# Optimization experiments

Measured on AMD Instinct MI355X. Metric: run time of the kernel, lower is better.

Reference implementation:

```python
import jax, jax.numpy as jnp
import numpy as np

ALPHA, BETA, LMBD, GAMMA = 0.0005, 1.0, 1.0, 1.0
MARGIN, THRES = 100.0, 0.5
EPS = 1e-7


def _bce(p, t):
    p = jnp.clip(p, EPS, 1.0 - EPS)
    return -jnp.mean(t * jnp.log(p) + (1.0 - t) * jnp.log1p(-p))


def setup_inputs() -> dict:
    key = jax.random.key(0)
    ks = jax.random.split(key, 9)
    B, T, D, C = 16, 2048, 2048, 100
    return {
        "score_act": jax.random.uniform(ks[0], (B, C), jnp.float32),
        "score_bkg": jax.random.uniform(ks[1], (B, C), jnp.float32),
        "feat_act": jax.random.normal(ks[2], (B, T, D), jnp.float32),
        "feat_bkg": jax.random.normal(ks[3], (B, T, D), jnp.float32),
        "label": jax.random.uniform(ks[4], (B, C), jnp.float32),
        "gt": jax.random.uniform(ks[5], (B, T, C), jnp.float32),
        "sup_cas": jax.random.uniform(ks[6], (B, T, C), jnp.float32),
        "cas_s": jax.random.uniform(ks[7], (B, T, C), jnp.float32),
        "cas_t": jax.random.uniform(ks[8], (B, T, C), jnp.float32),
    }


def reference(score_act, score_bkg, feat_act, feat_bkg, label, gt, sup_cas, cas_s, cas_t):
    # classification BCE against normalized multi-label target
    label_n = label / jnp.sum(label, axis=1, keepdims=True)
    loss_cls = _bce(score_act, label_n)

    # background BCE against uniform 1/C target
    C = label.shape[1]
    loss_be = _bce(score_bkg, jnp.full_like(label, 1.0 / C))

    # uncertainty modeling: feature-magnitude margin loss
    act_norm = jnp.linalg.norm(jnp.mean(feat_act, axis=1), axis=1)  # [B]
    bkg_norm = jnp.linalg.norm(jnp.mean(feat_bkg, axis=1), axis=1)  # [B]
    loss_act = jnp.maximum(MARGIN - act_norm, 0.0)
    loss_um = jnp.mean((loss_act + bkg_norm) ** 2)

    # balanced_ce, vectorized over (batch, class): mean of L2 norms over time
    # for (i,j) slices that contain at least one positive snippet
    pmask = (gt > THRES).astype(sup_cas.dtype)            # [B,T,C]
    norms = jnp.linalg.norm(sup_cas - pmask, axis=1)      # [B,C]
    valid = jnp.sum(pmask, axis=1) > 0                    # [B,C]
    count = jnp.maximum(jnp.sum(valid), 1).astype(norms.dtype)
    loss_sup = jnp.sum(jnp.where(valid, norms, 0.0)) / count

    # student/teacher CAS MSE
    loss_st = jnp.mean((cas_s - cas_t) ** 2)

    loss_total = (loss_cls + ALPHA * loss_um + BETA * loss_be
                  + LMBD * loss_sup + GAMMA * loss_st)
    return jnp.stack([loss_total, loss_cls, loss_be, loss_um, loss_sup, loss_st])
```

## Files before the change

kernel.cpp:

```cpp
#include <hip/hip_runtime.h>
#include <cmath>

constexpr int B = 16, T = 2048, D = 2048, C = 100;
#define EPS_F 1e-7f

__global__ void colsum_kernel(const float* __restrict__ feat, float* __restrict__ out,
                              int rows_per_chunk) {
    const int b = blockIdx.z;
    const int d0 = (blockIdx.x * blockDim.x + threadIdx.x) * 4;
    const int t0 = blockIdx.y * rows_per_chunk;
    float4 acc = make_float4(0.f, 0.f, 0.f, 0.f);
    const float* base = feat + ((size_t)b * T + t0) * D + d0;
    for (int t = 0; t < rows_per_chunk; ++t) {
        float4 v = *reinterpret_cast<const float4*>(base + (size_t)t * D);
        acc.x += v.x; acc.y += v.y; acc.z += v.z; acc.w += v.w;
    }
    float* o = out + b * D + d0;
    atomicAdd(o + 0, acc.x);
    atomicAdd(o + 1, acc.y);
    atomicAdd(o + 2, acc.z);
    atomicAdd(o + 3, acc.w);
}

__global__ void sup_kernel(const float* __restrict__ gt, const float* __restrict__ sup,
                           float* __restrict__ sumsq, float* __restrict__ cnt,
                           int rows_per_chunk) {
    const int b = blockIdx.y;
    const int c = threadIdx.x;
    const int t0 = blockIdx.x * rows_per_chunk;
    if (c >= C) return;
    float acc = 0.f, pc = 0.f;
    size_t base = ((size_t)b * T + t0) * C + c;
    for (int t = 0; t < rows_per_chunk; ++t) {
        float g = gt[base + (size_t)t * C];
        float s = sup[base + (size_t)t * C];
        float m = (g > 0.5f) ? 1.f : 0.f;
        float d = s - m;
        acc += d * d;
        pc += m;
    }
    atomicAdd(&sumsq[b * C + c], acc);
    atomicAdd(&cnt[b * C + c], pc);
}

__global__ void st_kernel(const float4* __restrict__ s, const float4* __restrict__ t,
                          float* __restrict__ acc, int n4) {
    int idx = blockIdx.x * blockDim.x + threadIdx.x;
    int stride = gridDim.x * blockDim.x;
    float local = 0.f;
    for (int i = idx; i < n4; i += stride) {
        float4 a = s[i], b4 = t[i];
        float dx = a.x - b4.x, dy = a.y - b4.y, dz = a.z - b4.z, dw = a.w - b4.w;
        local += dx * dx + dy * dy + dz * dz + dw * dw;
    }
    for (int off = 32; off; off >>= 1) local += __shfl_down(local, off, 64);
    __shared__ float wsum[4];
    int lane = threadIdx.x & 63, wv = threadIdx.x >> 6;
    if (lane == 0) wsum[wv] = local;
    __syncthreads();
    if (threadIdx.x == 0) {
        atomicAdd(acc, wsum[0] + wsum[1] + wsum[2] + wsum[3]);
    }
}

__device__ __forceinline__ float block_reduce256(float v, float* sdata) {
    int tid = threadIdx.x;
    sdata[tid] = v;
    __syncthreads();
    for (int s = 128; s > 0; s >>= 1) {
        if (tid < s) sdata[tid] += sdata[tid + s];
        __syncthreads();
    }
    float r = sdata[0];
    __syncthreads();
    return r;
}

__global__ void final_kernel(const float* __restrict__ score_act,
                             const float* __restrict__ score_bkg,
                             const float* __restrict__ label,
                             const float* __restrict__ colsum_act,
                             const float* __restrict__ colsum_bkg,
                             const float* __restrict__ sup_sumsq,
                             const float* __restrict__ sup_cnt,
                             const float* __restrict__ st_acc,
                             float* __restrict__ out) {
    __shared__ float sdata[256];
    __shared__ float rowsum[B];
    __shared__ float an[B], bn[B];
    const int tid = threadIdx.x;
    const int N = B * C;

    if (tid < B) rowsum[tid] = 0.f;
    __syncthreads();
    for (int i = tid; i < N; i += 256) atomicAdd(&rowsum[i / C], label[i]);
    __syncthreads();

    float lc = 0.f;
    for (int i = tid; i < N; i += 256) {
        float tgt = label[i] / rowsum[i / C];
        float p = fminf(fmaxf(score_act[i], EPS_F), 1.f - EPS_F);
        lc -= tgt * logf(p) + (1.f - tgt) * log1pf(-p);
    }
    float loss_cls = block_reduce256(lc, sdata) / (float)N;

    float lb = 0.f;
    const float u = 1.f / (float)C;
    for (int i = tid; i < N; i += 256) {
        float p = fminf(fmaxf(score_bkg[i], EPS_F), 1.f - EPS_F);
        lb -= u * logf(p) + (1.f - u) * log1pf(-p);
    }
    float loss_be = block_reduce256(lb, sdata) / (float)N;

    const float invT = 1.f / (float)T;
    for (int b = 0; b < B; ++b) {
        float la = 0.f, lg = 0.f;
        for (int d = tid; d < D; d += 256) {
            float va = colsum_act[b * D + d] * invT;
            float vb = colsum_bkg[b * D + d] * invT;
            la += va * va;
            lg += vb * vb;
        }
        float sa = block_reduce256(la, sdata);
        float sb = block_reduce256(lg, sdata);
        if (tid == 0) { an[b] = sqrtf(sa); bn[b] = sqrtf(sb); }
    }
    __syncthreads();

    float ss = 0.f, sc = 0.f;
    for (int i = tid; i < N; i += 256) {
        if (sup_cnt[i] > 0.f) { ss += sqrtf(sup_sumsq[i]); sc += 1.f; }
    }
    float sup_sum = block_reduce256(ss, sdata);
    float sup_count = block_reduce256(sc, sdata);

    if (tid == 0) {
        float loss_um = 0.f;
        for (int b = 0; b < B; ++b) {
            float la = fmaxf(100.f - an[b], 0.f);
            float v = la + bn[b];
            loss_um += v * v;
        }
        loss_um /= (float)B;
        float loss_sup = sup_sum / fmaxf(sup_count, 1.f);
        float loss_st = *st_acc / (float)((size_t)B * T * C);
        float total = loss_cls + 0.0005f * loss_um + 1.0f * loss_be
                    + 1.0f * loss_sup + 1.0f * loss_st;
        out[0] = total;
        out[1] = loss_cls;
        out[2] = loss_be;
        out[3] = loss_um;
        out[4] = loss_sup;
        out[5] = loss_st;
    }
}

extern "C" void kernel_launch(void* const* d_in, const int* in_sizes, int n_in,
                              void* d_out, int out_size, void* d_ws, size_t ws_size,
                              hipStream_t stream) {
    const float* score_act = (const float*)d_in[0];
    const float* score_bkg = (const float*)d_in[1];
    const float* feat_act  = (const float*)d_in[2];
    const float* feat_bkg  = (const float*)d_in[3];
    const float* label     = (const float*)d_in[4];
    const float* gt        = (const float*)d_in[5];
    const float* sup_cas   = (const float*)d_in[6];
    const float* cas_s     = (const float*)d_in[7];
    const float* cas_t     = (const float*)d_in[8];
    float* out = (float*)d_out;
    float* ws  = (float*)d_ws;

    float* colsum_act = ws;
    float* colsum_bkg = ws + (size_t)B * D;
    float* sup_sumsq  = ws + (size_t)2 * B * D;
    float* sup_cnt    = sup_sumsq + B * C;
    float* st_acc     = sup_cnt + B * C;
    size_t ws_needed  = ((size_t)2 * B * D + 2 * B * C + 1) * sizeof(float);

    hipMemsetAsync(d_ws, 0, ws_needed, stream);

    {
        const int rows = 64;
        dim3 grid(D / (256 * 4), T / rows, B);
        colsum_kernel<<<grid, 256, 0, stream>>>(feat_act, colsum_act, rows);
        colsum_kernel<<<grid, 256, 0, stream>>>(feat_bkg, colsum_bkg, rows);
    }
    {
        const int rows = 32;
        dim3 grid(T / rows, B);
        sup_kernel<<<grid, 128, 0, stream>>>(gt, sup_cas, sup_sumsq, sup_cnt, rows);
    }
    {
        int n4 = (B * T * C) / 4;
        st_kernel<<<1024, 256, 0, stream>>>((const float4*)cas_s, (const float4*)cas_t,
                                            st_acc, n4);
    }
    final_kernel<<<1, 256, 0, stream>>>(score_act, score_bkg, label,
                                        colsum_act, colsum_bkg,
                                        sup_sumsq, sup_cnt, st_acc, out);
}
```

Baseline: 660.9 us.

## Merge colsum launches, vectorize sup kernel, use nontemporal loads and shuffle reductions

Folds the two feature column-sum launches into one grid spanning both tensors. The supervision kernel is reworked to 256 threads with float4 loads across classes, 8 row groups per block and 64 rows per block. All streaming loads become nontemporal, and the final kernel's shared-memory tree reduction is replaced with wave shuffles. The aim is to cut launch overhead and raise effective bandwidth on the memory-bound reads; nontemporal hints may have no effect or may hurt on this hardware.

After: 664.5 us. Within noise of the previous version (+0.5%).

```diff
diff --git a/kernel.cpp b/kernel.cpp
--- a/kernel.cpp
+++ b/kernel.cpp
@@ -4,88 +4,106 @@
 constexpr int B = 16, T = 2048, D = 2048, C = 100;
 #define EPS_F 1e-7f
 
-__global__ void colsum_kernel(const float* __restrict__ feat, float* __restrict__ out,
-                              int rows_per_chunk) {
-    const int b = blockIdx.z;
-    const int d0 = (blockIdx.x * blockDim.x + threadIdx.x) * 4;
-    const int t0 = blockIdx.y * rows_per_chunk;
-    float4 acc = make_float4(0.f, 0.f, 0.f, 0.f);
+typedef float v4f __attribute__((ext_vector_type(4)));
+
+template <int ROWS>
+__global__ __launch_bounds__(256) void colsum_kernel(
+        const float* __restrict__ fa, const float* __restrict__ fb,
+        float* __restrict__ out) {
+    const int z = blockIdx.z;
+    const float* feat = (z < B) ? fa : fb;
+    const int b = (z < B) ? z : z - B;
+    const int d0 = (blockIdx.x * 256 + threadIdx.x) * 4;
+    const int t0 = blockIdx.y * ROWS;
     const float* base = feat + ((size_t)b * T + t0) * D + d0;
-    for (int t = 0; t < rows_per_chunk; ++t) {
-        float4 v = *reinterpret_cast<const float4*>(base + (size_t)t * D);
-        acc.x += v.x; acc.y += v.y; acc.z += v.z; acc.w += v.w;
-    }
-    float* o = out + b * D + d0;
+    v4f acc = (v4f)(0.f);
+#pragma unroll 8
+    for (int t = 0; t < ROWS; ++t) {
+        v4f v = __builtin_nontemporal_load(
+            reinterpret_cast<const v4f*>(base + (size_t)t * D));
+        acc += v;
+    }
+    float* o = out + (size_t)z * D + d0;
     atomicAdd(o + 0, acc.x);
     atomicAdd(o + 1, acc.y);
     atomicAdd(o + 2, acc.z);
     atomicAdd(o + 3, acc.w);
 }
 
-__global__ void sup_kernel(const float* __restrict__ gt, const float* __restrict__ sup,
-                           float* __restrict__ sumsq, float* __restrict__ cnt,
-                           int rows_per_chunk) {
+template <int ROWS>
+__global__ __launch_bounds__(256) void sup_kernel(
+        const float* __restrict__ gt, const float* __restrict__ sup,
+        float* __restrict__ sumsq, float* __restrict__ cnt) {
     const int b = blockIdx.y;
-    const int c = threadIdx.x;
-    const int t0 = blockIdx.x * rows_per_chunk;
-    if (c >= C) return;
-    float acc = 0.f, pc = 0.f;
-    size_t base = ((size_t)b * T + t0) * C + c;
-    for (int t = 0; t < rows_per_chunk; ++t) {
-        float g = gt[base + (size_t)t * C];
-        float s = sup[base + (size_t)t * C];
-        float m = (g > 0.5f) ? 1.f : 0.f;
-        float d = s - m;
-        acc += d * d;
-        pc += m;
-    }
-    atomicAdd(&sumsq[b * C + c], acc);
-    atomicAdd(&cnt[b * C + c], pc);
-}
-
-__global__ void st_kernel(const float4* __restrict__ s, const float4* __restrict__ t,
-                          float* __restrict__ acc, int n4) {
+    const int j = threadIdx.x & 31;
+    const int r = threadIdx.x >> 5;
+    if (j >= C / 4) return;
+    const int t0 = blockIdx.x * ROWS + r;
+    size_t base = ((size_t)b * T + t0) * C + 4 * j;
+    v4f acc = (v4f)(0.f);
+    v4f pc  = (v4f)(0.f);
+#pragma unroll
+    for (int t = 0; t < ROWS; t += 8) {
+        v4f g = __builtin_nontemporal_load(
+            reinterpret_cast<const v4f*>(gt  + base + (size_t)t * C));
+        v4f s = __builtin_nontemporal_load(
+            reinterpret_cast<const v4f*>(sup + base + (size_t)t * C));
+        float m, d;
+        m = (g.x > 0.5f) ? 1.f : 0.f; d = s.x - m; acc.x += d * d; pc.x += m;
+        m = (g.y > 0.5f) ? 1.f : 0.f; d = s.y - m; acc.y += d * d; pc.y += m;
+        m = (g.z > 0.5f) ? 1.f : 0.f; d = s.z - m; acc.z += d * d; pc.z += m;
+        m = (g.w > 0.5f) ? 1.f : 0.f; d = s.w - m; acc.w += d * d; pc.w += m;
+    }
+    float* sq = sumsq + b * C + 4 * j;
+    float* ct = cnt   + b * C + 4 * j;
+    atomicAdd(sq + 0, acc.x); atomicAdd(sq + 1, acc.y);
+    atomicAdd(sq + 2, acc.z); atomicAdd(sq + 3, acc.w);
+    atomicAdd(ct + 0, pc.x);  atomicAdd(ct + 1, pc.y);
+    atomicAdd(ct + 2, pc.z);  atomicAdd(ct + 3, pc.w);
+}
+
+__global__ __launch_bounds__(256) void st_kernel(
+        const float* __restrict__ s, const float* __restrict__ t,
+        float* __restrict__ acc, int n4) {
     int idx = blockIdx.x * blockDim.x + threadIdx.x;
     int stride = gridDim.x * blockDim.x;
     float local = 0.f;
     for (int i = idx; i < n4; i += stride) {
-        float4 a = s[i], b4 = t[i];
-        float dx = a.x - b4.x, dy = a.y - b4.y, dz = a.z - b4.z, dw = a.w - b4.w;
-        local += dx * dx + dy * dy + dz * dz + dw * dw;
+        v4f a  = __builtin_nontemporal_load(
+            reinterpret_cast<const v4f*>(s) + i);
+        v4f b4 = __builtin_nontemporal_load(
+            reinterpret_cast<const v4f*>(t) + i);
+        v4f d = a - b4;
+        local += d.x * d.x + d.y * d.y + d.z * d.z + d.w * d.w;
     }
     for (int off = 32; off; off >>= 1) local += __shfl_down(local, off, 64);
     __shared__ float wsum[4];
     int lane = threadIdx.x & 63, wv = threadIdx.x >> 6;
     if (lane == 0) wsum[wv] = local;
     __syncthreads();
-    if (threadIdx.x == 0) {
+    if (threadIdx.x == 0)
         atomicAdd(acc, wsum[0] + wsum[1] + wsum[2] + wsum[3]);
-    }
-}
-
-__device__ __forceinline__ float block_reduce256(float v, float* sdata) {
-    int tid = threadIdx.x;
-    sdata[tid] = v;
-    __syncthreads();
-    for (int s = 128; s > 0; s >>= 1) {
-        if (tid < s) sdata[tid] += sdata[tid + s];
-        __syncthreads();
-    }
-    float r = sdata[0];
-    __syncthreads();
-    return r;
-}
-
-__global__ void final_kernel(const float* __restrict__ score_act,
-                             const float* __restrict__ score_bkg,
-                             const float* __restrict__ label,
-                             const float* __restrict__ colsum_act,
-                             const float* __restrict__ colsum_bkg,
-                             const float* __restrict__ sup_sumsq,
-                             const float* __restrict__ sup_cnt,
-                             const float* __restrict__ st_acc,
-                             float* __restrict__ out) {
-    __shared__ float sdata[256];
+}
+
+__device__ __forceinline__ float block_reduce(float v, float* s4) {
+    for (int off = 32; off; off >>= 1) v += __shfl_down(v, off, 64);
+    int lane = threadIdx.x & 63, wv = threadIdx.x >> 6;
+    __syncthreads();
+    if (lane == 0) s4[wv] = v;
+    __syncthreads();
+    return s4[0] + s4[1] + s4[2] + s4[3];
+}
+
+__global__ __launch_bounds__(256) void final_kernel(
+        const float* __restrict__ score_act,
+        const float* __restrict__ score_bkg,
+        const float* __restrict__ label,
+        const float* __restrict__ colsum,
+        const float* __restrict__ sup_sumsq,
+        const float* __restrict__ sup_cnt,
+        const float* __restrict__ st_acc,
+        float* __restrict__ out) {
+    __shared__ float s4[4];
     __shared__ float rowsum[B];
     __shared__ float an[B], bn[B];
     const int tid = threadIdx.x;
@@ -102,7 +120,7 @@
         float p = fminf(fmaxf(score_act[i], EPS_F), 1.f - EPS_F);
         lc -= tgt * logf(p) + (1.f - tgt) * log1pf(-p);
     }
-    float loss_cls = block_reduce256(lc, sdata) / (float)N;
+    float loss_cls = block_reduce(lc, s4) / (float)N;
 
     float lb = 0.f;
     const float u = 1.f / (float)C;
@@ -110,19 +128,20 @@
         float p = fminf(fmaxf(score_bkg[i], EPS_F), 1.f - EPS_F);
         lb -= u * logf(p) + (1.f - u) * log1pf(-p);
     }
-    float loss_be = block_reduce256(lb, sdata) / (float)N;
+    float loss_be = block_reduce(lb, s4) / (float)N;
 
     const float invT = 1.f / (float)T;
+    const v4f* cs4 = reinterpret_cast<const v4f*>(colsum);
     for (int b = 0; b < B; ++b) {
         float la = 0.f, lg = 0.f;
-        for (int d = tid; d < D; d += 256) {
-            float va = colsum_act[b * D + d] * invT;
-            float vb = colsum_bkg[b * D + d] * invT;
-            la += va * va;
-            lg += vb * vb;
+        for (int i = tid; i < D / 4; i += 256) {
+            v4f va = cs4[(size_t)b * (D / 4) + i];
+            v4f vb = cs4[(size_t)(b + B) * (D / 4) + i];
+            la += (va.x * va.x + va.y * va.y + va.z * va.z + va.w * va.w) * invT * invT;
+            lg += (vb.x * vb.x + vb.y * vb.y + vb.z * vb.z + vb.w * vb.w) * invT * invT;
         }
-        float sa = block_reduce256(la, sdata);
-        float sb = block_reduce256(lg, sdata);
+        float sa = block_reduce(la, s4);
+        float sb = block_reduce(lg, s4);
         if (tid == 0) { an[b] = sqrtf(sa); bn[b] = sqrtf(sb); }
     }
     __syncthreads();
@@ -131,8 +150,8 @@
     for (int i = tid; i < N; i += 256) {
         if (sup_cnt[i] > 0.f) { ss += sqrtf(sup_sumsq[i]); sc += 1.f; }
     }
-    float sup_sum = block_reduce256(ss, sdata);
-    float sup_count = block_reduce256(sc, sdata);
+    float sup_sum   = block_reduce(ss, s4);
+    float sup_count = block_reduce(sc, s4);
 
     if (tid == 0) {
         float loss_um = 0.f;
@@ -170,32 +189,28 @@
     float* out = (float*)d_out;
     float* ws  = (float*)d_ws;
 
-    float* colsum_act = ws;
-    float* colsum_bkg = ws + (size_t)B * D;
-    float* sup_sumsq  = ws + (size_t)2 * B * D;
-    float* sup_cnt    = sup_sumsq + B * C;
-    float* st_acc     = sup_cnt + B * C;
-    size_t ws_needed  = ((size_t)2 * B * D + 2 * B * C + 1) * sizeof(float);
-
-    hipMemsetAsync(d_ws, 0, ws_needed, stream);
+    float* colsum    = ws;
+    float* sup_sumsq = ws + (size_t)2 * B * D;
+    float* sup_cnt   = sup_sumsq + B * C;
+    float* st_acc    = sup_cnt + B * C;
+    size_t ws_needed = ((size_t)2 * B * D + 2 * B * C + 1) * sizeof(float);
+
+    (void)hipMemsetAsync(d_ws, 0, ws_needed, stream);
 
     {
-        const int rows = 64;
-        dim3 grid(D / (256 * 4), T / rows, B);
-        colsum_kernel<<<grid, 256, 0, stream>>>(feat_act, colsum_act, rows);
-        colsum_kernel<<<grid, 256, 0, stream>>>(feat_bkg, colsum_bkg, rows);
+        constexpr int ROWS = 64;
+        dim3 grid(D / (256 * 4), T / ROWS, 2 * B);
+        colsum_kernel<ROWS><<<grid, 256, 0, stream>>>(feat_act, feat_bkg, colsum);
     }
     {
-        const int rows = 32;
-        dim3 grid(T / rows, B);
-        sup_kernel<<<grid, 128, 0, stream>>>(gt, sup_cas, sup_sumsq, sup_cnt, rows);
+        constexpr int ROWS = 64;
+        dim3 grid(T / ROWS, B);
+        sup_kernel<ROWS><<<grid, 256, 0, stream>>>(gt, sup_cas, sup_sumsq, sup_cnt);
     }
     {
         int n4 = (B * T * C) / 4;
-        st_kernel<<<1024, 256, 0, stream>>>((const float4*)cas_s, (const float4*)cas_t,
-                                            st_acc, n4);
+        st_kernel<<<1024, 256, 0, stream>>>(cas_s, cas_t, st_acc, n4);
     }
     final_kernel<<<1, 256, 0, stream>>>(score_act, score_bkg, label,
-                                        colsum_act, colsum_bkg,
-                                        sup_sumsq, sup_cnt, st_acc, out);
-}
+                                        colsum, sup_sumsq, sup_cnt, st_acc, out);
+}
```
